# Optimization experiments

Hardware: AMD Instinct MI355X
Metric: run time of the kernel (lower is better)

## Reference

```python
import jax, jax.numpy as jnp
import numpy as np

B, T, C, H = 2, 2048, 1024, 16
HD = C // H  # 64


def _rope(x, cos, sin):
    # x: [B, T, H, HD]; cos/sin: [T, HD//2]
    xr = x.reshape(*x.shape[:-1], HD // 2, 2)
    xre, xim = xr[..., 0], xr[..., 1]
    c = cos[None, :, None, :]
    s = sin[None, :, None, :]
    out_re = xre * c - xim * s
    out_im = xre * s + xim * c
    return jnp.stack([out_re, out_im], axis=-1).reshape(x.shape)


def setup_inputs() -> dict:
    key = jax.random.key(0)
    ks = jax.random.split(key, 4)
    x = jax.random.normal(ks[0], (B, T, C), dtype=jnp.float32)
    W_qkv = jax.random.normal(ks[1], (3 * C, C), dtype=jnp.float32) * (C ** -0.5)
    W_proj = jax.random.normal(ks[2], (C, C), dtype=jnp.float32) * (C ** -0.5)
    b_proj = jnp.zeros((C,), dtype=jnp.float32)
    # standard RoPE frequencies, theta=10000
    inv_freq = 1.0 / (10000.0 ** (np.arange(0, HD, 2, dtype=np.float32) / HD))
    angles = np.outer(np.arange(T, dtype=np.float32), inv_freq)  # [T, HD/2]
    freqs_cos = jnp.asarray(np.cos(angles), dtype=jnp.float32)
    freqs_sin = jnp.asarray(np.sin(angles), dtype=jnp.float32)
    return {"x": x, "freqs_cos": freqs_cos, "freqs_sin": freqs_sin,
            "W_qkv": W_qkv, "W_proj": W_proj, "b_proj": b_proj}


def reference(x, freqs_cos, freqs_sin, W_qkv, W_proj, b_proj):
    qkv = x @ W_qkv.T                       # [B, T, 3C]
    q, k, v = jnp.split(qkv, 3, axis=-1)
    q = q.reshape(B, T, H, HD)
    k = k.reshape(B, T, H, HD)
    v = v.reshape(B, T, H, HD)
    q = _rope(q, freqs_cos, freqs_sin)
    k = _rope(k, freqs_cos, freqs_sin)
    # [B, H, T, HD]
    q = q.transpose(0, 2, 1, 3)
    k = k.transpose(0, 2, 1, 3)
    v = v.transpose(0, 2, 1, 3)
    att = jnp.einsum('bhqd,bhkd->bhqk', q, k) * (HD ** -0.5)
    causal = jnp.tril(jnp.ones((T, T), dtype=bool))
    att = jnp.where(causal[None, None], att, -jnp.inf)
    att = jax.nn.softmax(att, axis=-1)
    out = jnp.einsum('bhqk,bhkd->bhqd', att, v)
    out = out.transpose(0, 2, 1, 3).reshape(B, T, C)
    return out @ W_proj.T + b_proj
```

## Files before the change

### kernel.cpp

```cpp
#include <hip/hip_runtime.h>


typedef short  bf16x8 __attribute__((ext_vector_type(8)));
typedef float  f32x4  __attribute__((ext_vector_type(4)));
typedef unsigned short u16x4 __attribute__((ext_vector_type(4)));

#define B_  2
#define T_  2048
#define H_  16
#define HD_ 64
#define NINF (-__builtin_inff())

static __device__ __forceinline__ unsigned short f2bf(float f) {
    union { float f; unsigned u; } v; v.f = f;
    unsigned r = v.u + 0x7fffu + ((v.u >> 16) & 1u);
    return (unsigned short)(r >> 16);
}

#define GLOAD_LDS16(gp, lp)                                                              \
    __builtin_amdgcn_global_load_lds((const __attribute__((address_space(1))) void*)(gp), \
                                     (__attribute__((address_space(3))) void*)(lp), 16, 0, 0)

__global__ void convert2(const float* __restrict__ x, const float* __restrict__ wqkv,
                         unsigned short* __restrict__ xb, unsigned short* __restrict__ wqkvb) {
    int i = blockIdx.x * blockDim.x + threadIdx.x;
    const float* src; unsigned short* dst; int off;
    if (i < 1048576) { src = x;    dst = xb;    off = i; }
    else             { src = wqkv; dst = wqkvb; off = i - 1048576; }
    float4 f = ((const float4*)src)[off];
    u16x4 o; o[0] = f2bf(f.x); o[1] = f2bf(f.y); o[2] = f2bf(f.z); o[3] = f2bf(f.w);
    ((u16x4*)dst)[off] = o;
}

__global__ __launch_bounds__(256) void gemm_qkv(const unsigned short* __restrict__ A,
                                                const unsigned short* __restrict__ Bm,
                                                const float* __restrict__ fa,
                                                const float* __restrict__ fb,
                                                unsigned short* __restrict__ Qo,
                                                unsigned short* __restrict__ Ko,
                                                unsigned short* __restrict__ Vt,
                                                const float* __restrict__ wproj,
                                                unsigned short* __restrict__ wprojb) {
    __shared__ __align__(16) unsigned short As[128 * 64];
    __shared__ __align__(16) unsigned short Bs[128 * 64];
    const int bid = blockIdx.x;
    if (bid >= 768) {
        int base = (bid - 768) * 256 + threadIdx.x;
#pragma unroll
        for (int k = 0; k < 16; k++) {
            int u = base + k * 16384;
            float4 f = ((const float4*)wproj)[u];
            u16x4 o; o[0] = f2bf(f.x); o[1] = f2bf(f.y); o[2] = f2bf(f.z); o[3] = f2bf(f.w);
            ((u16x4*)wprojb)[u] = o;
        }
        return;
    }

    const int K = 1024;
    const int tid  = threadIdx.x;
    const int w    = tid >> 6;
    const int lane = tid & 63;
    const int r    = lane & 15, g = lane >> 4;

    const int xcd  = bid & 7;
    const int i_   = bid >> 3;
    const int m0   = ((xcd >> 1) * 8 + i_ / 12) * 128;
    const int n0   = ((xcd & 1) * 12 + i_ % 12) * 128;
    const int wm   = (w >> 1) * 64, wn = (w & 1) * 64;

    f32x4 acc[4][4];
#pragma unroll
    for (int i = 0; i < 4; i++)
#pragma unroll
        for (int j = 0; j < 4; j++) acc[i][j] = (f32x4){0.f, 0.f, 0.f, 0.f};

    const int rowS = tid >> 3;
    const int csS  = (tid & 7) ^ (rowS & 7);
    const int t8e  = tid * 8;
    const unsigned short* ga = A  + (size_t)(m0 + rowS) * K + csS * 8;
    const unsigned short* gb = Bm + (size_t)(n0 + rowS) * K + csS * 8;

    int roff[4][2];
#pragma unroll
    for (int mi = 0; mi < 4; mi++)
#pragma unroll
        for (int kk = 0; kk < 2; kk++)
            roff[mi][kk] = (mi * 16 + r) * 64 + (((4 * kk + g) ^ (r & 7)) * 8);

    for (int k0 = 0; k0 < K; k0 += 64) {
        __syncthreads();
        GLOAD_LDS16(ga + k0,            &As[t8e]);
        GLOAD_LDS16(ga + 32 * K + k0,   &As[2048 + t8e]);
        GLOAD_LDS16(ga + 64 * K + k0,   &As[4096 + t8e]);
        GLOAD_LDS16(ga + 96 * K + k0,   &As[6144 + t8e]);
        GLOAD_LDS16(gb + k0,            &Bs[t8e]);
        GLOAD_LDS16(gb + 32 * K + k0,   &Bs[2048 + t8e]);
        GLOAD_LDS16(gb + 64 * K + k0,   &Bs[4096 + t8e]);
        GLOAD_LDS16(gb + 96 * K + k0,   &Bs[6144 + t8e]);
        __syncthreads();

#pragma unroll
        for (int kk = 0; kk < 2; kk++) {
            bf16x8 a[4], b[4];
#pragma unroll
            for (int mi = 0; mi < 4; mi++) a[mi] = *(const bf16x8*)&As[wm * 64 + roff[mi][kk]];
#pragma unroll
            for (int ni = 0; ni < 4; ni++) b[ni] = *(const bf16x8*)&Bs[wn * 64 + roff[ni][kk]];
#pragma unroll
            for (int mi = 0; mi < 4; mi++)
#pragma unroll
                for (int ni = 0; ni < 4; ni++)
                    acc[mi][ni] = __builtin_amdgcn_mfma_f32_16x16x32_bf16(a[mi], b[ni], acc[mi][ni], 0, 0, 0);
        }
    }

    const float* fcos = (fa[0] > 0.5f) ? fa : fb;
    const float* fsin = (fa[0] > 0.5f) ? fb : fa;
    const int region = n0 >> 10;

    if (region < 2) {
        unsigned short* dst = region ? Ko : Qo;
        const float sgn = (r & 1) ? 1.f : -1.f;
#pragma unroll
        for (int mi = 0; mi < 4; mi++) {
            int row0 = m0 + wm + mi * 16 + 4 * g;
            int b    = row0 >> 11;
            int t0   = row0 & 2047;
#pragma unroll
            for (int ni = 0; ni < 4; ni++) {
                int nn = (n0 & 1023) + wn + ni * 16 + r;
                int h  = nn >> 6, dd = nn & 63;
                int i  = dd >> 1;
                size_t obase = ((size_t)((b * 16 + h) * 2048 + t0)) * 64 + dd;
#pragma unroll
                for (int j = 0; j < 4; j++) {
                    float c = fcos[(t0 + j) * 32 + i];
                    float s = fsin[(t0 + j) * 32 + i];
                    float v  = acc[mi][ni][j];
                    float vp = __shfl_xor(v, 1);
                    float out = __builtin_fmaf(sgn * vp, s, v * c);
                    dst[obase + (size_t)j * 64] = f2bf(out);
                }
            }
        }
    } else {
#pragma unroll
        for (int mi = 0; mi < 4; mi++) {
            int row0 = m0 + wm + mi * 16 + 4 * g;
            int b    = row0 >> 11;
            int t0   = row0 & 2047;
            int tp   = (t0 & ~31) + 8 * ((t0 & 15) >> 2) + 4 * ((t0 & 31) >> 4);
#pragma unroll
            for (int ni = 0; ni < 4; ni++) {
                int nn = (n0 & 1023) + wn + ni * 16 + r;
                int h  = nn >> 6, dd = nn & 63;
                u16x4 ov;
#pragma unroll
                for (int j = 0; j < 4; j++) ov[j] = f2bf(acc[mi][ni][j]);
                *(u16x4*)(Vt + ((size_t)((b * 16 + h) * 64 + dd)) * 2048 + tp) = ov;
            }
        }
    }
}

__global__ __launch_bounds__(256) void gemm_nt(const unsigned short* __restrict__ A,
                                               const unsigned short* __restrict__ Bm,
                                               float* __restrict__ Cm,
                                               const float* __restrict__ bias,
                                               int M, int N, int K) {
    __shared__ __align__(16) unsigned short As[128 * 64];
    __shared__ __align__(16) unsigned short Bs[128 * 64];
    const int tid  = threadIdx.x;
    const int w    = tid >> 6;
    const int lane = tid & 63;
    const int r    = lane & 15, g = lane >> 4;

    const int bid  = blockIdx.x;
    const int xcd  = bid & 7;
    const int i_   = bid >> 3;
    const int m0   = ((xcd >> 1) * 8 + (i_ >> 2)) * 128;
    const int n0   = ((xcd & 1) * 4 + (i_ & 3)) * 128;
    const int wm   = (w >> 1) * 64, wn = (w & 1) * 64;

    f32x4 acc[4][4];
#pragma unroll
    for (int i = 0; i < 4; i++)
#pragma unroll
        for (int j = 0; j < 4; j++) acc[i][j] = (f32x4){0.f, 0.f, 0.f, 0.f};

    const int rowS = tid >> 3;
    const int csS  = (tid & 7) ^ (rowS & 7);
    const int t8e  = tid * 8;
    const unsigned short* ga = A  + (size_t)(m0 + rowS) * K + csS * 8;
    const unsigned short* gb = Bm + (size_t)(n0 + rowS) * K + csS * 8;

    int roff[4][2];
#pragma unroll
    for (int mi = 0; mi < 4; mi++)
#pragma unroll
        for (int kk = 0; kk < 2; kk++)
            roff[mi][kk] = (mi * 16 + r) * 64 + (((4 * kk + g) ^ (r & 7)) * 8);

    for (int k0 = 0; k0 < K; k0 += 64) {
        __syncthreads();
        GLOAD_LDS16(ga + k0,            &As[t8e]);
        GLOAD_LDS16(ga + 32 * K + k0,   &As[2048 + t8e]);
        GLOAD_LDS16(ga + 64 * K + k0,   &As[4096 + t8e]);
        GLOAD_LDS16(ga + 96 * K + k0,   &As[6144 + t8e]);
        GLOAD_LDS16(gb + k0,            &Bs[t8e]);
        GLOAD_LDS16(gb + 32 * K + k0,   &Bs[2048 + t8e]);
        GLOAD_LDS16(gb + 64 * K + k0,   &Bs[4096 + t8e]);
        GLOAD_LDS16(gb + 96 * K + k0,   &Bs[6144 + t8e]);
        __syncthreads();

#pragma unroll
        for (int kk = 0; kk < 2; kk++) {
            bf16x8 a[4], b[4];
#pragma unroll
            for (int mi = 0; mi < 4; mi++) a[mi] = *(const bf16x8*)&As[wm * 64 + roff[mi][kk]];
#pragma unroll
            for (int ni = 0; ni < 4; ni++) b[ni] = *(const bf16x8*)&Bs[wn * 64 + roff[ni][kk]];
#pragma unroll
            for (int mi = 0; mi < 4; mi++)
#pragma unroll
                for (int ni = 0; ni < 4; ni++)
                    acc[mi][ni] = __builtin_amdgcn_mfma_f32_16x16x32_bf16(a[mi], b[ni], acc[mi][ni], 0, 0, 0);
        }
    }

#pragma unroll
    for (int mi = 0; mi < 4; mi++) {
        int row = m0 + wm + mi * 16 + 4 * g;
#pragma unroll
        for (int ni = 0; ni < 4; ni++) {
            int col = n0 + wn + ni * 16 + r;
            float bv = bias[col];
#pragma unroll
            for (int j = 0; j < 4; j++)
                Cm[(size_t)(row + j) * N + col] = acc[mi][ni][j] + bv;
        }
    }
}

template <bool DIAG>
static __device__ __forceinline__ void softmax128(const f32x4 s[8], int key0, int qrow,
                                                  float& m, float& l,
                                                  f32x4 o[4], bf16x8 pf[4], int g) {
    const float SCL = 0.125f * 1.4426950408889634f;
    float sv[32];
#pragma unroll
    for (int ks = 0; ks < 8; ks++)
#pragma unroll
        for (int j = 0; j < 4; j++) {
            float x = s[ks][j];
            if (DIAG && (key0 + ks * 16 + 4 * g + j > qrow)) x = NINF;
            sv[ks * 4 + j] = x;
        }
    float t16[16];
#pragma unroll
    for (int i = 0; i < 16; i++) t16[i] = fmaxf(sv[i], sv[i + 16]);
#pragma unroll
    for (int i = 0; i < 8; i++) t16[i] = fmaxf(t16[i], t16[i + 8]);
#pragma unroll
    for (int i = 0; i < 4; i++) t16[i] = fmaxf(t16[i], t16[i + 4]);
    float tm = fmaxf(fmaxf(t16[0], t16[1]), fmaxf(t16[2], t16[3]));
    tm = fmaxf(tm, __shfl_xor(tm, 16));
    tm = fmaxf(tm, __shfl_xor(tm, 32));

    float msc;
    if (__all(tm <= m)) {
        msc = m * SCL;
    } else {
        float mnew  = fmaxf(m, tm);
        float alpha = __builtin_amdgcn_exp2f((m - mnew) * SCL);
        l *= alpha;
#pragma unroll
        for (int ch = 0; ch < 4; ch++) o[ch] *= alpha;
        m = mnew;
        msc = mnew * SCL;
    }
    float p[32];
#pragma unroll
    for (int i = 0; i < 32; i++) p[i] = __builtin_amdgcn_exp2f(__builtin_fmaf(sv[i], SCL, -msc));
    float ps = 0.f;
#pragma unroll
    for (int i = 0; i < 32; i += 4) ps += ((p[i] + p[i + 1]) + (p[i + 2] + p[i + 3]));
    l += ps;
#pragma unroll
    for (int kb = 0; kb < 4; kb++) {
        union { unsigned w[4]; bf16x8 v; } u;
        asm("v_cvt_pk_bf16_f32 %0, %1, %2" : "=v"(u.w[0]) : "v"(p[8 * kb + 0]), "v"(p[8 * kb + 1]));
        asm("v_cvt_pk_bf16_f32 %0, %1, %2" : "=v"(u.w[1]) : "v"(p[8 * kb + 2]), "v"(p[8 * kb + 3]));
        asm("v_cvt_pk_bf16_f32 %0, %1, %2" : "=v"(u.w[2]) : "v"(p[8 * kb + 4]), "v"(p[8 * kb + 5]));
        asm("v_cvt_pk_bf16_f32 %0, %1, %2" : "=v"(u.w[3]) : "v"(p[8 * kb + 6]), "v"(p[8 * kb + 7]));
        pf[kb] = u.v;
    }
}

__global__ __launch_bounds__(256, 4) void attn_fwd(const unsigned short* __restrict__ Q,
                                                   const unsigned short* __restrict__ Kk,
                                                   const unsigned short* __restrict__ Vt,
                                                   unsigned short* __restrict__ O) {
    __shared__ __align__(16) unsigned short Ks[2][8192];
    __shared__ __align__(16) unsigned short Vs[2][8192];

    const int w    = threadIdx.x >> 6;
    const int lane = threadIdx.x & 63;
    const int l15  = lane & 15, g = lane >> 4;

    const int bid = blockIdx.x;
    const int x   = bid & 7;
    const int y   = (bid >> 3) & 31;
    const int q   = bid >> 8;
    const int bh  = x | ((y & 3) << 3);
    const int z   = y >> 2;
    const int r   = (q == 0) ? z : (q == 1) ? 15 - z : (q == 2) ? 16 + z : 31 - z;
    const int b   = bh >> 4, h = bh & 15;

    const unsigned short* Qb = Q  + (size_t)bh * T_ * HD_;
    const unsigned short* Kb = Kk + (size_t)bh * T_ * HD_;
    const unsigned short* Vb = Vt + (size_t)bh * HD_ * T_;

    const int qrow = r * 64 + 16 * w + l15;
    bf16x8 qf0 = *(const bf16x8*)(Qb + (size_t)qrow * 64 + 8 * g);
    bf16x8 qf1 = *(const bf16x8*)(Qb + (size_t)qrow * 64 + 32 + 8 * g);

    f32x4 o[4];
#pragma unroll
    for (int ch = 0; ch < 4; ch++) o[ch] = (f32x4){0, 0, 0, 0};
    float m2 = NINF, lsum = 0.f;

    int koff[8][2];
#pragma unroll
    for (int i = 0; i < 8; i++) {
        int row = 16 * i + l15;
        koff[i][0] = row * 128 + ((g ^ (row & 7)) << 4);
        koff[i][1] = row * 128 + (((4 + g) ^ (row & 7)) << 4);
    }
    int voff[4][4];
#pragma unroll
    for (int ch = 0; ch < 4; ch++) {
        int row = 16 * ch + l15;
#pragma unroll
        for (int kb = 0; kb < 4; kb++)
            voff[ch][kb] = row * 256 + (((kb * 4 + g) ^ (row & 7)) << 4);
    }

    const int t   = threadIdx.x;
    const int rK0 = t >> 3;
    const int csK = (t & 7) ^ (rK0 & 7);
    const int rV0 = t >> 4;
    const int csV = (t & 15) ^ (rV0 & 7);
    const int t8e = t * 8;
    const unsigned short* sK = Kb + (size_t)rK0 * 64 + csK * 8;
    const unsigned short* sV = Vb + (size_t)rV0 * 2048 + csV * 8;

#define STAGE_TILE(bb, key0_)                                                     \
    do {                                                                          \
        GLOAD_LDS16(sK + (size_t)(key0_) * 64,         &Ks[bb][t8e]);             \
        GLOAD_LDS16(sK + (size_t)(key0_) * 64 + 2048,  &Ks[bb][2048 + t8e]);      \
        GLOAD_LDS16(sK + (size_t)(key0_) * 64 + 4096,  &Ks[bb][4096 + t8e]);      \
        GLOAD_LDS16(sK + (size_t)(key0_) * 64 + 6144,  &Ks[bb][6144 + t8e]);      \
        GLOAD_LDS16(sV + (key0_),                      &Vs[bb][t8e]);             \
        GLOAD_LDS16(sV + (key0_) + 32768,              &Vs[bb][2048 + t8e]);      \
        GLOAD_LDS16(sV + (key0_) + 65536,              &Vs[bb][4096 + t8e]);      \
        GLOAD_LDS16(sV + (key0_) + 98304,              &Vs[bb][6144 + t8e]);      \
    } while (0)

    const int ktEnd = r >> 1;
    STAGE_TILE(0, 0);
    __syncthreads();

    for (int kt = 0; kt <= ktEnd; ++kt) {
        const int key0 = kt * 128;
        const int cur  = kt & 1;
        if (kt < ktEnd) STAGE_TILE(cur ^ 1, key0 + 128);

        const char* KsB = (const char*)&Ks[cur][0];
        const char* VsB = (const char*)&Vs[cur][0];

        f32x4 z4 = (f32x4){0, 0, 0, 0};
        f32x4 s[8];
        __builtin_amdgcn_s_setprio(1);
#pragma unroll
        for (int ks = 0; ks < 8; ks++) {
            bf16x8 kf0 = *(const bf16x8*)(KsB + koff[ks][0]);
            bf16x8 kf1 = *(const bf16x8*)(KsB + koff[ks][1]);
            s[ks] = __builtin_amdgcn_mfma_f32_16x16x32_bf16(kf0, qf0, z4, 0, 0, 0);
            s[ks] = __builtin_amdgcn_mfma_f32_16x16x32_bf16(kf1, qf1, s[ks], 0, 0, 0);
        }
        __builtin_amdgcn_s_setprio(0);

        bf16x8 pf[4];
        if (kt == ktEnd) softmax128<true >(s, key0, qrow, m2, lsum, o, pf, g);
        else             softmax128<false>(s, key0, qrow, m2, lsum, o, pf, g);

        __builtin_amdgcn_s_setprio(1);
#pragma unroll
        for (int ch = 0; ch < 4; ch++) {
            bf16x8 v0 = *(const bf16x8*)(VsB + voff[ch][0]);
            bf16x8 v1 = *(const bf16x8*)(VsB + voff[ch][1]);
            bf16x8 v2 = *(const bf16x8*)(VsB + voff[ch][2]);
            bf16x8 v3 = *(const bf16x8*)(VsB + voff[ch][3]);
            o[ch] = __builtin_amdgcn_mfma_f32_16x16x32_bf16(v0, pf[0], o[ch], 0, 0, 0);
            o[ch] = __builtin_amdgcn_mfma_f32_16x16x32_bf16(v1, pf[1], o[ch], 0, 0, 0);
            o[ch] = __builtin_amdgcn_mfma_f32_16x16x32_bf16(v2, pf[2], o[ch], 0, 0, 0);
            o[ch] = __builtin_amdgcn_mfma_f32_16x16x32_bf16(v3, pf[3], o[ch], 0, 0, 0);
        }
        __builtin_amdgcn_s_setprio(0);

        __syncthreads();
    }
#undef STAGE_TILE

    lsum += __shfl_xor(lsum, 16);
    lsum += __shfl_xor(lsum, 32);
    float inv = 1.f / lsum;

    size_t obase = (((size_t)b * T_ + qrow) * H_ + h) * HD_;
#pragma unroll
    for (int ch = 0; ch < 4; ch++) {
        int d0 = 16 * ch + 4 * g;
        u16x4 ov;
#pragma unroll
        for (int jj = 0; jj < 4; jj++) ov[jj] = f2bf(o[ch][jj] * inv);
        *(u16x4*)(O + obase + d0) = ov;
    }
}

extern "C" void kernel_launch(void* const* d_in, const int* in_sizes, int n_in,
                              void* d_out, int out_size, void* d_ws, size_t ws_size,
                              hipStream_t stream) {
    (void)out_size;
    const float *x = nullptr, *wqkv = nullptr, *wproj = nullptr, *bproj = nullptr;
    const float *fa = nullptr, *fb = nullptr;
    for (int i = 0; i < n_in; i++) {
        switch (in_sizes[i]) {
            case 4194304: x     = (const float*)d_in[i]; break;
            case 3145728: wqkv  = (const float*)d_in[i]; break;
            case 1048576: wproj = (const float*)d_in[i]; break;
            case 1024:    bproj = (const float*)d_in[i]; break;
            case 65536:   if (!fa) fa = (const float*)d_in[i]; else fb = (const float*)d_in[i]; break;
            default: break;
        }
    }
    if (!x || !wqkv || !wproj || !bproj || !fa || !fb) return;
    if (ws_size < (size_t)48 * 1024 * 1024) return;

    char* ws = (char*)d_ws;
    const size_t MB = 1024 * 1024;
    unsigned short* xb     = (unsigned short*)(ws);
    unsigned short* wqkvb  = (unsigned short*)(ws + 8  * MB);
    unsigned short* wprojb = (unsigned short*)(ws + 14 * MB);
    unsigned short* qro    = (unsigned short*)(ws + 16 * MB);
    unsigned short* kro    = (unsigned short*)(ws + 24 * MB);
    unsigned short* vt     = (unsigned short*)(ws + 32 * MB);
    unsigned short* oat    = (unsigned short*)(ws + 40 * MB);

    convert2<<<7168, 256, 0, stream>>>(x, wqkv, xb, wqkvb);

    gemm_qkv<<<832, 256, 0, stream>>>(xb, wqkvb, fa, fb, qro, kro, vt, wproj, wprojb);

    attn_fwd<<<1024, 256, 0, stream>>>(qro, kro, vt, oat);

    gemm_nt<<<256, 256, 0, stream>>>(oat, wprojb, (float*)d_out, bproj,
                                     4096, 1024, 1024);
}
```

Before: 118.8 us.

## Load V fragments directly from global into registers instead of staging through LDS

Removes the double-buffered LDS staging of the transposed V tile. Each wave now loads its V fragments straight from global memory into registers at the start of each key tile, ahead of the QK^T and softmax work, so the load latency can hide behind that compute. This halves LDS use and drops the LDS reads for V. In exchange, the four waves in a block, which share the same keys, each fetch the same V data separately, and register pressure rises. The launch-bounds occupancy hint drops from 4 to 2 and the setprio hints are removed.

```diff
diff --git a/kernel.cpp b/kernel.cpp
--- a/kernel.cpp
+++ b/kernel.cpp
@@ -297,12 +297,11 @@
     }
 }
 
-__global__ __launch_bounds__(256, 4) void attn_fwd(const unsigned short* __restrict__ Q,
+__global__ __launch_bounds__(256, 2) void attn_fwd(const unsigned short* __restrict__ Q,
                                                    const unsigned short* __restrict__ Kk,
                                                    const unsigned short* __restrict__ Vt,
                                                    unsigned short* __restrict__ O) {
     __shared__ __align__(16) unsigned short Ks[2][8192];
-    __shared__ __align__(16) unsigned short Vs[2][8192];
 
     const int w    = threadIdx.x >> 6;
     const int lane = threadIdx.x & 63;
@@ -337,51 +336,46 @@
         koff[i][0] = row * 128 + ((g ^ (row & 7)) << 4);
         koff[i][1] = row * 128 + (((4 + g) ^ (row & 7)) << 4);
     }
-    int voff[4][4];
-#pragma unroll
-    for (int ch = 0; ch < 4; ch++) {
-        int row = 16 * ch + l15;
-#pragma unroll
-        for (int kb = 0; kb < 4; kb++)
-            voff[ch][kb] = row * 256 + (((kb * 4 + g) ^ (row & 7)) << 4);
-    }
+
+    const unsigned short* vchp[4];
+#pragma unroll
+    for (int ch = 0; ch < 4; ch++)
+        vchp[ch] = Vb + (size_t)(16 * ch + l15) * 2048 + 8 * g;
 
     const int t   = threadIdx.x;
     const int rK0 = t >> 3;
     const int csK = (t & 7) ^ (rK0 & 7);
-    const int rV0 = t >> 4;
-    const int csV = (t & 15) ^ (rV0 & 7);
     const int t8e = t * 8;
     const unsigned short* sK = Kb + (size_t)rK0 * 64 + csK * 8;
-    const unsigned short* sV = Vb + (size_t)rV0 * 2048 + csV * 8;
-
-#define STAGE_TILE(bb, key0_)                                                     \
+
+#define STAGE_K(bb, key0_)                                                        \
     do {                                                                          \
         GLOAD_LDS16(sK + (size_t)(key0_) * 64,         &Ks[bb][t8e]);             \
         GLOAD_LDS16(sK + (size_t)(key0_) * 64 + 2048,  &Ks[bb][2048 + t8e]);      \
         GLOAD_LDS16(sK + (size_t)(key0_) * 64 + 4096,  &Ks[bb][4096 + t8e]);      \
         GLOAD_LDS16(sK + (size_t)(key0_) * 64 + 6144,  &Ks[bb][6144 + t8e]);      \
-        GLOAD_LDS16(sV + (key0_),                      &Vs[bb][t8e]);             \
-        GLOAD_LDS16(sV + (key0_) + 32768,              &Vs[bb][2048 + t8e]);      \
-        GLOAD_LDS16(sV + (key0_) + 65536,              &Vs[bb][4096 + t8e]);      \
-        GLOAD_LDS16(sV + (key0_) + 98304,              &Vs[bb][6144 + t8e]);      \
     } while (0)
 
     const int ktEnd = r >> 1;
-    STAGE_TILE(0, 0);
+    STAGE_K(0, 0);
     __syncthreads();
 
     for (int kt = 0; kt <= ktEnd; ++kt) {
         const int key0 = kt * 128;
         const int cur  = kt & 1;
-        if (kt < ktEnd) STAGE_TILE(cur ^ 1, key0 + 128);
+
+        bf16x8 va[4][4];
+#pragma unroll
+        for (int ch = 0; ch < 4; ch++)
+#pragma unroll
+            for (int kb = 0; kb < 4; kb++)
+                va[ch][kb] = *(const bf16x8*)(vchp[ch] + key0 + 32 * kb);
+
+        if (kt < ktEnd) STAGE_K(cur ^ 1, key0 + 128);
 
         const char* KsB = (const char*)&Ks[cur][0];
-        const char* VsB = (const char*)&Vs[cur][0];
-
         f32x4 z4 = (f32x4){0, 0, 0, 0};
         f32x4 s[8];
-        __builtin_amdgcn_s_setprio(1);
 #pragma unroll
         for (int ks = 0; ks < 8; ks++) {
             bf16x8 kf0 = *(const bf16x8*)(KsB + koff[ks][0]);
@@ -389,29 +383,22 @@
             s[ks] = __builtin_amdgcn_mfma_f32_16x16x32_bf16(kf0, qf0, z4, 0, 0, 0);
             s[ks] = __builtin_amdgcn_mfma_f32_16x16x32_bf16(kf1, qf1, s[ks], 0, 0, 0);
         }
-        __builtin_amdgcn_s_setprio(0);
 
         bf16x8 pf[4];
         if (kt == ktEnd) softmax128<true >(s, key0, qrow, m2, lsum, o, pf, g);
         else             softmax128<false>(s, key0, qrow, m2, lsum, o, pf, g);
 
-        __builtin_amdgcn_s_setprio(1);
 #pragma unroll
         for (int ch = 0; ch < 4; ch++) {
-            bf16x8 v0 = *(const bf16x8*)(VsB + voff[ch][0]);
-            bf16x8 v1 = *(const bf16x8*)(VsB + voff[ch][1]);
-            bf16x8 v2 = *(const bf16x8*)(VsB + voff[ch][2]);
-            bf16x8 v3 = *(const bf16x8*)(VsB + voff[ch][3]);
-            o[ch] = __builtin_amdgcn_mfma_f32_16x16x32_bf16(v0, pf[0], o[ch], 0, 0, 0);
-            o[ch] = __builtin_amdgcn_mfma_f32_16x16x32_bf16(v1, pf[1], o[ch], 0, 0, 0);
-            o[ch] = __builtin_amdgcn_mfma_f32_16x16x32_bf16(v2, pf[2], o[ch], 0, 0, 0);
-            o[ch] = __builtin_amdgcn_mfma_f32_16x16x32_bf16(v3, pf[3], o[ch], 0, 0, 0);
-        }
-        __builtin_amdgcn_s_setprio(0);
+            o[ch] = __builtin_amdgcn_mfma_f32_16x16x32_bf16(va[ch][0], pf[0], o[ch], 0, 0, 0);
+            o[ch] = __builtin_amdgcn_mfma_f32_16x16x32_bf16(va[ch][1], pf[1], o[ch], 0, 0, 0);
+            o[ch] = __builtin_amdgcn_mfma_f32_16x16x32_bf16(va[ch][2], pf[2], o[ch], 0, 0, 0);
+            o[ch] = __builtin_amdgcn_mfma_f32_16x16x32_bf16(va[ch][3], pf[3], o[ch], 0, 0, 0);
+        }
 
         __syncthreads();
     }
-#undef STAGE_TILE
+#undef STAGE_K
 
     lsum += __shfl_xor(lsum, 16);
     lsum += __shfl_xor(lsum, 32);
```

After: 149.4 us. 25.7% more time.
